# Performance work log

Hardware: AMD Instinct MI355X
Metric: run time of the kernel (lower is better)

The kernel has to match this reference:

```python
import jax, jax.numpy as jnp
import numpy as np

DIM = 128
NUM_HEADS = 2
WS = 8  # window_size


def setup_inputs() -> dict:
    key = jax.random.key(0)
    ks = jax.random.split(key, 8)
    B, C, H, W = 1, DIM, 64, 128  # W must equal DIM (proj acts on last spatial axis)
    w_scale = 1.0 / np.sqrt(DIM)
    return {
        "x": jax.random.normal(ks[0], (B, C, H, W), jnp.float32),
        "wavelet_features": jax.random.normal(ks[1], (B, C, H, W), jnp.float32),
        "Wq": jax.random.normal(ks[2], (DIM, DIM), jnp.float32) * w_scale,
        "bq": jnp.zeros((DIM,), jnp.float32),
        "Wk": jax.random.normal(ks[3], (DIM, DIM), jnp.float32) * w_scale,
        "bk": jnp.zeros((DIM,), jnp.float32),
        "Wv": jax.random.normal(ks[4], (DIM, DIM), jnp.float32) * w_scale,
        "bv": jnp.zeros((DIM,), jnp.float32),
        "Wp": jax.random.normal(ks[5], (DIM, DIM), jnp.float32) * w_scale,
        "bp": jnp.zeros((DIM,), jnp.float32),
    }


def _window_partition(t):
    # 'b c (h wh) (w ww) -> b (h w) (wh ww) c'
    B, C, H, W = t.shape
    h, w = H // WS, W // WS
    t = t.reshape(B, C, h, WS, w, WS)
    t = t.transpose(0, 2, 4, 3, 5, 1)  # B,h,w,wh,ww,C
    return t.reshape(B, h * w, WS * WS, C)


def reference(x, wavelet_features, Wq, bq, Wk, bk, Wv, bv, Wp, bp):
    B, C, H, W = x.shape
    hd = C // NUM_HEADS
    scale = hd ** (-0.5)

    xw = _window_partition(x)                   # [B, nW, ws*ws, C]
    ww = _window_partition(wavelet_features)    # [B, nW, ws*ws, C]

    q = xw @ Wq.T + bq
    k = ww @ Wk.T + bk
    v = ww @ Wv.T + bv

    # NOTE: original code flattens windows+tokens together, so attention is
    # GLOBAL over all N = H*W tokens (window partition is just a permutation).
    N = q.shape[1] * q.shape[2]
    q = q.reshape(B, N, NUM_HEADS, hd).transpose(0, 2, 1, 3)  # [B,h,N,d]
    k = k.reshape(B, N, NUM_HEADS, hd).transpose(0, 2, 1, 3)
    v = v.reshape(B, N, NUM_HEADS, hd).transpose(0, 2, 1, 3)

    attn = jax.nn.softmax(jnp.einsum('bhnd,bhmd->bhnm', q, k) * scale, axis=-1)
    out = jnp.einsum('bhnm,bhmd->bhnd', attn, v)  # [B,h,N,d]
    out = out.transpose(0, 2, 1, 3).reshape(B, N, C)

    # 'b (h w) (wh ww) c -> b c (h wh) (w ww)'
    h, w = H // WS, W // WS
    out = out.reshape(B, h, w, WS, WS, C).transpose(0, 5, 1, 3, 2, 4).reshape(B, C, H, W)

    # Faithful quirk: proj Linear acts on the LAST axis (spatial W == dim).
    out = out @ Wp.T + bp
    return out
```

## Files before the change

### kernel.cpp

```cpp
#include <hip/hip_runtime.h>
#include <stdint.h>

typedef float    f32x4  __attribute__((ext_vector_type(4)));
typedef __bf16   bf16x8 __attribute__((ext_vector_type(8)));
typedef short    s16x8  __attribute__((ext_vector_type(8)));
typedef int      i32x4  __attribute__((ext_vector_type(4)));
typedef unsigned short u16x4 __attribute__((ext_vector_type(4)));

#define DEVINL __device__ __forceinline__

DEVINL unsigned short f2bf(float f) {
  unsigned u = __builtin_bit_cast(unsigned, f);
  return (unsigned short)((u + 0x7fffu + ((u >> 16) & 1u)) >> 16);
}

DEVINL f32x4 mfma16(bf16x8 a, bf16x8 b, f32x4 c) {
  return __builtin_amdgcn_mfma_f32_16x16x32_bf16(a, b, c, 0, 0, 0);
}

DEVINL bf16x8 lds_frag(const unsigned char* p) {
  return __builtin_bit_cast(bf16x8, *(const s16x8*)p);
}

template <int CTRL>
DEVINL float dppf(float x) {
  int xi = __builtin_bit_cast(int, x);
  return __builtin_bit_cast(float, __builtin_amdgcn_update_dpp(xi, xi, CTRL, 0xF, 0xF, true));
}
DEVINL float redmax16(float v) {
  v = fmaxf(v, dppf<0xB1>(v));
  v = fmaxf(v, dppf<0x4E>(v));
  v = fmaxf(v, dppf<0x141>(v));
  v = fmaxf(v, dppf<0x140>(v));
  return v;
}

__global__ __launch_bounds__(256) void prep_w_kernel(
    const float* __restrict__ wq, const float* __restrict__ wk,
    const float* __restrict__ wv, const float* __restrict__ wp,
    unsigned short* __restrict__ wbf) {
  int id = blockIdx.x * 256 + threadIdx.x;
  int m = id >> 12;
  const float* src = (m == 0) ? wq : (m == 1) ? wk : (m == 2) ? wv : wp;
  f32x4 v = ((const f32x4*)src)[id & 4095];
  u16x4 o;
  o[0] = f2bf(v[0]); o[1] = f2bf(v[1]); o[2] = f2bf(v[2]); o[3] = f2bf(v[3]);
  ((u16x4*)wbf)[id] = o;
}

__global__ __launch_bounds__(256) void qkv_kernel(
    const float* __restrict__ x, const float* __restrict__ wav,
    const unsigned short* __restrict__ wbf,
    const float* __restrict__ bq, const float* __restrict__ bk, const float* __restrict__ bv,
    unsigned short* __restrict__ Qb, unsigned short* __restrict__ Kb,
    unsigned short* __restrict__ Vt) {
  __shared__ __align__(16) unsigned char sm[32768];
  const int tid = threadIdx.x;
  const int g = blockIdx.x >> 7;
  const int s0 = (blockIdx.x & 127) * 64;
  const float* srcm = (g == 0) ? x : wav;

  {
    const int c = tid >> 1, half = tid & 1;
    const float* xs = srcm + c * 8192 + s0 + half * 32;
#pragma unroll
    for (int i = 0; i < 8; ++i) {
      f32x4 vx = *(const f32x4*)(xs + i * 4);
#pragma unroll
      for (int j = 0; j < 4; ++j) {
        int s = half * 32 + i * 4 + j;
        int off = (c * 2) ^ ((s & 7) << 4);
        *(unsigned short*)(sm + s * 256 + off) = f2bf(vx[j]);
      }
    }
  }
  __syncthreads();

  const int w = tid >> 6, l = tid & 63, lr = l & 15, lh = l >> 4;
  const int arow = w * 16 + lr;
  const int aswz = (lr & 7) << 4;

  const unsigned char* asrc = sm + arow * 256;
  const unsigned char* wsrc = (const unsigned char*)wbf + g * 32768;
  f32x4 acc[8];
#pragma unroll
  for (int jt = 0; jt < 8; ++jt) acc[jt] = (f32x4){0.f, 0.f, 0.f, 0.f};
#pragma unroll
  for (int ks = 0; ks < 4; ++ks) {
    bf16x8 a = lds_frag(asrc + ((ks * 64 + lh * 16) ^ aswz));
#pragma unroll
    for (int jt = 0; jt < 8; ++jt) {
      bf16x8 bb = __builtin_bit_cast(
          bf16x8, *(const s16x8*)(wsrc + (jt * 16 + lr) * 256 + ks * 64 + lh * 16));
      acc[jt] = mfma16(a, bb, acc[jt]);
    }
  }
  if (g < 2) {
    const float* bias = g ? bk : bq;
    unsigned short* outp = g ? Kb : Qb;
#pragma unroll
    for (int jt = 0; jt < 8; ++jt) {
      float bb = bias[jt * 16 + lr];
#pragma unroll
      for (int r = 0; r < 4; ++r) {
        int row = s0 + w * 16 + lh * 4 + r;
        outp[row * 128 + jt * 16 + lr] = f2bf(acc[jt][r] + bb);
      }
    }
  } else {
    unsigned char* sm2 = sm + 16384;
#pragma unroll
    for (int jt = 0; jt < 8; ++jt) {
      float bb = bv[jt * 16 + lr];
#pragma unroll
      for (int r = 0; r < 4; ++r) {
        int jj = jt * 16 + lr;
        int sl = w * 16 + lh * 4 + r;
        *(unsigned short*)(sm2 + jj * 128 + ((sl * 2) ^ ((jj & 7) << 4))) =
            f2bf(acc[jt][r] + bb);
      }
    }
    __syncthreads();
#pragma unroll
    for (int g2 = 0; g2 < 4; ++g2) {
      int jj = w * 32 + g2 * 8 + (l >> 3);
      s16x8 row = *(const s16x8*)(sm2 + jj * 128 + (((l & 7) * 16) ^ ((jj & 7) << 4)));
      *(s16x8*)(Vt + jj * 8192 + s0 + (l & 7) * 8) = row;
    }
  }
}

__global__ __launch_bounds__(256) void attn_kernel(
    const unsigned short* __restrict__ Qb, const unsigned short* __restrict__ Kb,
    const unsigned short* __restrict__ Vt, float* __restrict__ Opart,
    float* __restrict__ Ml, float* __restrict__ Ll, int NIT) {
  __shared__ __align__(16) unsigned char sm[32768];
  const int tid = threadIdx.x;
  const int bid = blockIdx.x;
  const int sp = bid >> 7, g = bid & 127;
  const int h = g & 1, qb2 = g >> 1;
  const int q0 = qb2 * 128;
  const int t0 = sp * NIT;
  const int w = tid >> 6, l = tid & 63, lr = l & 15, lh = l >> 4;
  const int lswz = (lr & 7) << 4;

  bf16x8 qfA[2], qfB[2];
#pragma unroll
  for (int ks = 0; ks < 2; ++ks) {
    qfA[ks] = __builtin_bit_cast(
        bf16x8, *(const s16x8*)(Qb + (q0 + w * 16 + lr) * 128 + h * 64 + ks * 32 + lh * 8));
    qfB[ks] = __builtin_bit_cast(
        bf16x8, *(const s16x8*)(Qb + (q0 + 64 + w * 16 + lr) * 128 + h * 64 + ks * 32 + lh * 8));
  }

  const s16x8 ones_i = {0x3F80, 0x3F80, 0x3F80, 0x3F80, 0x3F80, 0x3F80, 0x3F80, 0x3F80};
  const bf16x8 onesf = __builtin_bit_cast(bf16x8, ones_i);

  f32x4 accA[4], accB[4];
  float mA[4], lA[4], mB[4], lB[4];
#pragma unroll
  for (int i = 0; i < 4; ++i) {
    accA[i] = (f32x4){0.f,0.f,0.f,0.f}; accB[i] = (f32x4){0.f,0.f,0.f,0.f};
    mA[i] = -1e30f; lA[i] = 0.f; mB[i] = -1e30f; lB[i] = 0.f;
  }

  int srow[2], soff[2], sldsoff[2];
#pragma unroll
  for (int i = 0; i < 2; ++i) {
    int ch = tid + i * 256;
    srow[i] = ch >> 3;
    soff[i] = (ch & 7) * 8;
    sldsoff[i] = srow[i] * 128 + ((soff[i] * 2) ^ ((srow[i] & 7) << 4));
  }

  {
#pragma unroll
    for (int i = 0; i < 2; ++i) {
      i32x4 kv = *(const i32x4*)(Kb + (t0 * 64 + srow[i]) * 128 + h * 64 + soff[i]);
      i32x4 vv = *(const i32x4*)(Vt + (h * 64 + srow[i]) * 8192 + t0 * 64 + soff[i]);
      *(i32x4*)(sm + sldsoff[i]) = kv;
      *(i32x4*)(sm + 8192 + sldsoff[i]) = vv;
    }
  }
  __syncthreads();

  const float sc = 0.18033688011112042f;

  for (int tt = 0; tt < NIT; ++tt) {
    const int t = t0 + tt;
    i32x4 nk[2], nv[2];
    if (tt < NIT - 1) {
#pragma unroll
      for (int i = 0; i < 2; ++i) {
        nk[i] = *(const i32x4*)(Kb + ((t + 1) * 64 + srow[i]) * 128 + h * 64 + soff[i]);
        nv[i] = *(const i32x4*)(Vt + (h * 64 + srow[i]) * 8192 + (t + 1) * 64 + soff[i]);
      }
    }
    const unsigned char* kb = sm;
    const unsigned char* vb = sm + 8192;
    unsigned char* pbA = sm + 16384;
    unsigned char* pbB = sm + 24576;

    f32x4 sA[4], sB[4];
#pragma unroll
    for (int nt = 0; nt < 4; ++nt) { sA[nt] = (f32x4){0.f,0.f,0.f,0.f}; sB[nt] = (f32x4){0.f,0.f,0.f,0.f}; }
#pragma unroll
    for (int ks = 0; ks < 2; ++ks) {
#pragma unroll
      for (int nt = 0; nt < 4; ++nt) {
        bf16x8 kf = lds_frag(kb + (nt * 16 + lr) * 128 + ((ks * 64 + lh * 16) ^ lswz));
        sA[nt] = mfma16(qfA[ks], kf, sA[nt]);
        sB[nt] = mfma16(qfB[ks], kf, sB[nt]);
      }
    }

#pragma unroll
    for (int r = 0; r < 4; ++r) {
      float mx = fmaxf(fmaxf(sA[0][r], sA[1][r]), fmaxf(sA[2][r], sA[3][r]));
      mx = redmax16(mx) * sc;
      float mn = fmaxf(mA[r], mx);
      float al = __builtin_amdgcn_exp2f(mA[r] - mn);
      mA[r] = mn;
      lA[r] *= al;
#pragma unroll
      for (int nt = 0; nt < 4; ++nt)
        sA[nt][r] = __builtin_amdgcn_exp2f(fmaf(sA[nt][r], sc, -mn));
#pragma unroll
      for (int ct = 0; ct < 4; ++ct) accA[ct][r] *= al;
    }
#pragma unroll
    for (int r = 0; r < 4; ++r) {
      float mx = fmaxf(fmaxf(sB[0][r], sB[1][r]), fmaxf(sB[2][r], sB[3][r]));
      mx = redmax16(mx) * sc;
      float mn = fmaxf(mB[r], mx);
      float al = __builtin_amdgcn_exp2f(mB[r] - mn);
      mB[r] = mn;
      lB[r] *= al;
#pragma unroll
      for (int nt = 0; nt < 4; ++nt)
        sB[nt][r] = __builtin_amdgcn_exp2f(fmaf(sB[nt][r], sc, -mn));
#pragma unroll
      for (int ct = 0; ct < 4; ++ct) accB[ct][r] *= al;
    }

    const int qrow = w * 16 + lh * 4;
#pragma unroll
    for (int r = 0; r < 4; r += 2) {
      int qa = qrow + r, qb = qrow + r + 1;
      int swza = (qa & 7) << 4, swzb = (qb & 7) << 4;
#pragma unroll
      for (int nt = 0; nt < 4; ++nt) {
        int koff = (nt * 16 + lr) * 2;
        unsigned u;
        asm("v_cvt_pk_bf16_f32 %0, %1, %2" : "=v"(u) : "v"(sA[nt][r]), "v"(sA[nt][r + 1]));
        *(unsigned short*)(pbA + qa * 128 + (koff ^ swza)) = (unsigned short)u;
        *(unsigned short*)(pbA + qb * 128 + (koff ^ swzb)) = (unsigned short)(u >> 16);
        asm("v_cvt_pk_bf16_f32 %0, %1, %2" : "=v"(u) : "v"(sB[nt][r]), "v"(sB[nt][r + 1]));
        *(unsigned short*)(pbB + qa * 128 + (koff ^ swza)) = (unsigned short)u;
        *(unsigned short*)(pbB + qb * 128 + (koff ^ swzb)) = (unsigned short)(u >> 16);
      }
    }
    asm volatile("s_waitcnt lgkmcnt(0)" ::: "memory");
    __builtin_amdgcn_sched_barrier(0);

    bf16x8 paA[2], paB[2];
#pragma unroll
    for (int ks = 0; ks < 2; ++ks) {
      paA[ks] = lds_frag(pbA + (w * 16 + lr) * 128 + ((ks * 64 + lh * 16) ^ lswz));
      paB[ks] = lds_frag(pbB + (w * 16 + lr) * 128 + ((ks * 64 + lh * 16) ^ lswz));
    }
    f32x4 ltA = (f32x4){0.f,0.f,0.f,0.f}, ltB = (f32x4){0.f,0.f,0.f,0.f};
#pragma unroll
    for (int ks = 0; ks < 2; ++ks) {
      ltA = mfma16(paA[ks], onesf, ltA);
      ltB = mfma16(paB[ks], onesf, ltB);
#pragma unroll
      for (int ct = 0; ct < 4; ++ct) {
        bf16x8 vf = lds_frag(vb + (ct * 16 + lr) * 128 + ((ks * 64 + lh * 16) ^ lswz));
        accA[ct] = mfma16(paA[ks], vf, accA[ct]);
        accB[ct] = mfma16(paB[ks], vf, accB[ct]);
      }
    }
#pragma unroll
    for (int r = 0; r < 4; ++r) { lA[r] += ltA[r]; lB[r] += ltB[r]; }

    __syncthreads();
    if (tt < NIT - 1) {
#pragma unroll
      for (int i = 0; i < 2; ++i) {
        *(i32x4*)(sm + sldsoff[i]) = nk[i];
        *(i32x4*)(sm + 8192 + sldsoff[i]) = nv[i];
      }
    }
    __syncthreads();
  }

  const size_t pbA_i = (size_t)sp * 256 + 4 * qb2 + h;
  const size_t pbB_i = (size_t)sp * 256 + 4 * qb2 + 2 + h;
  float* opA = Opart + pbA_i * 4096;
  float* opB = Opart + pbB_i * 4096;
#pragma unroll
  for (int ct = 0; ct < 4; ++ct) {
#pragma unroll
    for (int r = 0; r < 4; ++r) {
      int q = w * 16 + lh * 4 + r;
      opA[q * 64 + ct * 16 + lr] = accA[ct][r];
      opB[q * 64 + ct * 16 + lr] = accB[ct][r];
    }
  }
  if (lr == 0) {
#pragma unroll
    for (int r = 0; r < 4; ++r) {
      int q = w * 16 + lh * 4 + r;
      Ml[pbA_i * 64 + q] = mA[r];
      Ll[pbA_i * 64 + q] = lA[r];
      Ml[pbB_i * 64 + q] = mB[r];
      Ll[pbB_i * 64 + q] = lB[r];
    }
  }
}

__global__ __launch_bounds__(256) void combine_kernel(
    const float* __restrict__ Opart, const float* __restrict__ Ml,
    const float* __restrict__ Ll, unsigned short* __restrict__ Ot, int S) {
  __shared__ float wgt_s[8][32];
  __shared__ float rinv_s[32];
  __shared__ unsigned short lt[64][34];
  const int bid = blockIdx.x;
  const int hq = bid >> 1, half = bid & 1;
  const int h = hq & 1, q0 = (hq >> 1) * 64;
  const int t = threadIdx.x;

  if (t < 32) {
    int qg = half * 32 + t;
    float m8[8];
    float M = -1e30f;
    for (int sp = 0; sp < S; ++sp) {
      m8[sp] = Ml[(size_t)(sp * 256 + hq) * 64 + qg];
      M = fmaxf(M, m8[sp]);
    }
    float L = 0.f;
    for (int sp = 0; sp < S; ++sp) {
      float wv = __builtin_amdgcn_exp2f(m8[sp] - M);
      wgt_s[sp][t] = wv;
      L += Ll[(size_t)(sp * 256 + hq) * 64 + qg] * wv;
    }
    rinv_s[t] = 1.0f / L;
  }
  __syncthreads();

  const int q = t >> 3;
  const int dc = t & 7;
  const int qg = half * 32 + q;
  f32x4 o0 = (f32x4){0.f,0.f,0.f,0.f}, o1 = (f32x4){0.f,0.f,0.f,0.f};
  for (int sp = 0; sp < S; ++sp) {
    const f32x4* src =
        (const f32x4*)(Opart + (size_t)(sp * 256 + hq) * 4096 + qg * 64 + dc * 8);
    float wv = wgt_s[sp][q];
    o0 += src[0] * wv;
    o1 += src[1] * wv;
  }
  float rinv = rinv_s[q];
#pragma unroll
  for (int j = 0; j < 4; ++j) lt[dc * 8 + j][q] = f2bf(o0[j] * rinv);
#pragma unroll
  for (int j = 0; j < 4; ++j) lt[dc * 8 + 4 + j][q] = f2bf(o1[j] * rinv);
  __syncthreads();

  const int d = t >> 2, q8 = (t & 3) * 8;
  unsigned short tmp[8];
#pragma unroll
  for (int j = 0; j < 8; ++j) tmp[j] = lt[d][q8 + j];
  *(s16x8*)(Ot + (size_t)(h * 64 + d) * 8192 + q0 + half * 32 + q8) = *(s16x8*)tmp;
}

__global__ __launch_bounds__(256) void proj_kernel(
    const unsigned short* __restrict__ Ot, const unsigned short* __restrict__ wbf,
    const float* __restrict__ bp, float* __restrict__ out) {
  __shared__ __align__(16) unsigned char sm[16384];
  const int tid = threadIdx.x;
  const int r0 = blockIdx.x * 64;
#pragma unroll
  for (int i = 0; i < 4; ++i) {
    int chk = tid + 256 * i;
    i32x4 v = *(const i32x4*)(Ot + r0 * 128 + chk * 8);
    int row = chk >> 4, off = (chk & 15) * 16;
    *(i32x4*)(sm + row * 256 + (off ^ ((row & 7) << 4))) = v;
  }
  __syncthreads();
  const int w = tid >> 6, l = tid & 63, lr = l & 15, lh = l >> 4;
  f32x4 acc[8];
#pragma unroll
  for (int jt = 0; jt < 8; ++jt) acc[jt] = (f32x4){0.f, 0.f, 0.f, 0.f};
  const unsigned char* wsrc = (const unsigned char*)wbf + 3 * 32768;
#pragma unroll
  for (int ks = 0; ks < 4; ++ks) {
    bf16x8 a = lds_frag(sm + (w * 16 + lr) * 256 + ((ks * 64 + lh * 16) ^ ((lr & 7) << 4)));
#pragma unroll
    for (int jt = 0; jt < 8; ++jt) {
      bf16x8 bb = __builtin_bit_cast(
          bf16x8, *(const s16x8*)(wsrc + (jt * 16 + lr) * 256 + ks * 64 + lh * 16));
      acc[jt] = mfma16(a, bb, acc[jt]);
    }
  }
#pragma unroll
  for (int jt = 0; jt < 8; ++jt) {
    float bb = bp[jt * 16 + lr];
#pragma unroll
    for (int r = 0; r < 4; ++r)
      out[(r0 + w * 16 + lh * 4 + r) * 128 + jt * 16 + lr] = acc[jt][r] + bb;
  }
}

extern "C" void kernel_launch(void* const* d_in, const int* in_sizes, int n_in,
                              void* d_out, int out_size, void* d_ws, size_t ws_size,
                              hipStream_t stream) {
  const float* x   = (const float*)d_in[0];
  const float* wav = (const float*)d_in[1];
  const float* Wq  = (const float*)d_in[2];
  const float* bq  = (const float*)d_in[3];
  const float* Wk  = (const float*)d_in[4];
  const float* bk  = (const float*)d_in[5];
  const float* Wv  = (const float*)d_in[6];
  const float* bv  = (const float*)d_in[7];
  const float* Wp  = (const float*)d_in[8];
  const float* bp  = (const float*)d_in[9];
  (void)in_sizes; (void)n_in; (void)out_size;

  unsigned char* ws = (unsigned char*)d_ws;
  unsigned short* Qb  = (unsigned short*)(ws);
  unsigned short* Kb  = (unsigned short*)(ws + 2097152);
  unsigned short* Vt  = (unsigned short*)(ws + 4194304);
  unsigned short* Ot  = (unsigned short*)(ws + 6291456);
  unsigned short* Wbf = (unsigned short*)(ws + 8388608);

  const size_t pbase = 8519680;
  int S = 8;
  while (S > 1 && pbase + (size_t)S * 4325376 > ws_size) S >>= 1;
  float* Opart = (float*)(ws + pbase);
  float* Ml    = (float*)(ws + pbase + (size_t)S * 4194304);
  float* Ll    = (float*)(ws + pbase + (size_t)S * 4194304 + (size_t)S * 65536);
  const int NIT = 128 / S;

  prep_w_kernel<<<64, 256, 0, stream>>>(Wq, Wk, Wv, Wp, Wbf);
  qkv_kernel<<<384, 256, 0, stream>>>(x, wav, Wbf, bq, bk, bv, Qb, Kb, Vt);
  attn_kernel<<<128 * S, 256, 0, stream>>>(Qb, Kb, Vt, Opart, Ml, Ll, NIT);
  combine_kernel<<<512, 256, 0, stream>>>(Opart, Ml, Ll, Ot, S);
  proj_kernel<<<128, 256, 0, stream>>>(Ot, Wbf, bp, (float*)d_out);
}
```

Measured before the change: 123.1 us.

## Double key tile to 128 per iteration and alias P buffers over K

The attention loop now handles 128 keys per iteration instead of 64, halving the iteration count and the per-iteration barriers and softmax rescales. The P buffers now overlap the K panel region, which needs an extra barrier after the S computation, and the next-tile global prefetch moves later in the iteration. The larger score tile raises register pressure and LDS use grows to 48KB, which may cut occupancy.

```diff
diff --git a/kernel.cpp b/kernel.cpp
--- a/kernel.cpp
+++ b/kernel.cpp
@@ -134,7 +134,7 @@
     const unsigned short* __restrict__ Qb, const unsigned short* __restrict__ Kb,
     const unsigned short* __restrict__ Vt, float* __restrict__ Opart,
     float* __restrict__ Ml, float* __restrict__ Ll, int NIT) {
-  __shared__ __align__(16) unsigned char sm[32768];
+  __shared__ __align__(16) unsigned char sm[49152];
   const int tid = threadIdx.x;
   const int bid = blockIdx.x;
   const int sp = bid >> 7, g = bid & 127;
@@ -164,22 +164,27 @@
     mA[i] = -1e30f; lA[i] = 0.f; mB[i] = -1e30f; lB[i] = 0.f;
   }
 
-  int srow[2], soff[2], sldsoff[2];
-#pragma unroll
-  for (int i = 0; i < 2; ++i) {
+  int kglob[4], kldsoff[4], vglob[4], vldsoff[4];
+#pragma unroll
+  for (int i = 0; i < 4; ++i) {
     int ch = tid + i * 256;
-    srow[i] = ch >> 3;
-    soff[i] = (ch & 7) * 8;
-    sldsoff[i] = srow[i] * 128 + ((soff[i] * 2) ^ ((srow[i] & 7) << 4));
+    int key = ch >> 3, slot = ch & 7;
+    int kr = key & 63;
+    kldsoff[i] = (key >> 6) * 8192 + kr * 128 + ((slot * 16) ^ ((kr & 7) << 4));
+    kglob[i] = key * 128 + h * 64 + slot * 8;
+    int d = ch >> 4, kslot = ch & 15;
+    vldsoff[i] = 16384 + (kslot >> 3) * 8192 + d * 128 +
+                 (((kslot & 7) * 16) ^ ((d & 7) << 4));
+    vglob[i] = (h * 64 + d) * 8192 + kslot * 8;
   }
 
   {
 #pragma unroll
-    for (int i = 0; i < 2; ++i) {
-      i32x4 kv = *(const i32x4*)(Kb + (t0 * 64 + srow[i]) * 128 + h * 64 + soff[i]);
-      i32x4 vv = *(const i32x4*)(Vt + (h * 64 + srow[i]) * 8192 + t0 * 64 + soff[i]);
-      *(i32x4*)(sm + sldsoff[i]) = kv;
-      *(i32x4*)(sm + 8192 + sldsoff[i]) = vv;
+    for (int i = 0; i < 4; ++i) {
+      i32x4 kv = *(const i32x4*)(Kb + (size_t)t0 * 16384 + kglob[i]);
+      i32x4 vv = *(const i32x4*)(Vt + (size_t)t0 * 128 + vglob[i]);
+      *(i32x4*)(sm + kldsoff[i]) = kv;
+      *(i32x4*)(sm + vldsoff[i]) = vv;
     }
   }
   __syncthreads();
@@ -187,61 +192,54 @@
   const float sc = 0.18033688011112042f;
 
   for (int tt = 0; tt < NIT; ++tt) {
-    const int t = t0 + tt;
-    i32x4 nk[2], nv[2];
-    if (tt < NIT - 1) {
-#pragma unroll
-      for (int i = 0; i < 2; ++i) {
-        nk[i] = *(const i32x4*)(Kb + ((t + 1) * 64 + srow[i]) * 128 + h * 64 + soff[i]);
-        nv[i] = *(const i32x4*)(Vt + (h * 64 + srow[i]) * 8192 + (t + 1) * 64 + soff[i]);
-      }
-    }
-    const unsigned char* kb = sm;
-    const unsigned char* vb = sm + 8192;
-    unsigned char* pbA = sm + 16384;
-    unsigned char* pbB = sm + 24576;
-
-    f32x4 sA[4], sB[4];
-#pragma unroll
-    for (int nt = 0; nt < 4; ++nt) { sA[nt] = (f32x4){0.f,0.f,0.f,0.f}; sB[nt] = (f32x4){0.f,0.f,0.f,0.f}; }
+    f32x4 sA8[8], sB8[8];
+#pragma unroll
+    for (int nt = 0; nt < 8; ++nt) { sA8[nt] = (f32x4){0.f,0.f,0.f,0.f}; sB8[nt] = (f32x4){0.f,0.f,0.f,0.f}; }
 #pragma unroll
     for (int ks = 0; ks < 2; ++ks) {
 #pragma unroll
-      for (int nt = 0; nt < 4; ++nt) {
-        bf16x8 kf = lds_frag(kb + (nt * 16 + lr) * 128 + ((ks * 64 + lh * 16) ^ lswz));
-        sA[nt] = mfma16(qfA[ks], kf, sA[nt]);
-        sB[nt] = mfma16(qfB[ks], kf, sB[nt]);
+      for (int nt = 0; nt < 8; ++nt) {
+        bf16x8 kf = lds_frag(sm + (nt >> 2) * 8192 + ((nt & 3) * 16 + lr) * 128 +
+                             ((ks * 64 + lh * 16) ^ lswz));
+        sA8[nt] = mfma16(qfA[ks], kf, sA8[nt]);
+        sB8[nt] = mfma16(qfB[ks], kf, sB8[nt]);
       }
     }
 
 #pragma unroll
     for (int r = 0; r < 4; ++r) {
-      float mx = fmaxf(fmaxf(sA[0][r], sA[1][r]), fmaxf(sA[2][r], sA[3][r]));
+      float mx = sA8[0][r];
+#pragma unroll
+      for (int nt = 1; nt < 8; ++nt) mx = fmaxf(mx, sA8[nt][r]);
       mx = redmax16(mx) * sc;
       float mn = fmaxf(mA[r], mx);
       float al = __builtin_amdgcn_exp2f(mA[r] - mn);
       mA[r] = mn;
       lA[r] *= al;
 #pragma unroll
-      for (int nt = 0; nt < 4; ++nt)
-        sA[nt][r] = __builtin_amdgcn_exp2f(fmaf(sA[nt][r], sc, -mn));
+      for (int nt = 0; nt < 8; ++nt)
+        sA8[nt][r] = __builtin_amdgcn_exp2f(fmaf(sA8[nt][r], sc, -mn));
 #pragma unroll
       for (int ct = 0; ct < 4; ++ct) accA[ct][r] *= al;
     }
 #pragma unroll
     for (int r = 0; r < 4; ++r) {
-      float mx = fmaxf(fmaxf(sB[0][r], sB[1][r]), fmaxf(sB[2][r], sB[3][r]));
+      float mx = sB8[0][r];
+#pragma unroll
+      for (int nt = 1; nt < 8; ++nt) mx = fmaxf(mx, sB8[nt][r]);
       mx = redmax16(mx) * sc;
       float mn = fmaxf(mB[r], mx);
       float al = __builtin_amdgcn_exp2f(mB[r] - mn);
       mB[r] = mn;
       lB[r] *= al;
 #pragma unroll
-      for (int nt = 0; nt < 4; ++nt)
-        sB[nt][r] = __builtin_amdgcn_exp2f(fmaf(sB[nt][r], sc, -mn));
+      for (int nt = 0; nt < 8; ++nt)
+        sB8[nt][r] = __builtin_amdgcn_exp2f(fmaf(sB8[nt][r], sc, -mn));
 #pragma unroll
       for (int ct = 0; ct < 4; ++ct) accB[ct][r] *= al;
     }
+
+    __syncthreads();
 
     const int qrow = w * 16 + lh * 4;
 #pragma unroll
@@ -249,34 +247,47 @@
       int qa = qrow + r, qb = qrow + r + 1;
       int swza = (qa & 7) << 4, swzb = (qb & 7) << 4;
 #pragma unroll
-      for (int nt = 0; nt < 4; ++nt) {
-        int koff = (nt * 16 + lr) * 2;
+      for (int nt = 0; nt < 8; ++nt) {
+        int pbase = (nt >> 2) * 8192;
+        int koff = (nt & 3) * 32 + lr * 2;
         unsigned u;
-        asm("v_cvt_pk_bf16_f32 %0, %1, %2" : "=v"(u) : "v"(sA[nt][r]), "v"(sA[nt][r + 1]));
-        *(unsigned short*)(pbA + qa * 128 + (koff ^ swza)) = (unsigned short)u;
-        *(unsigned short*)(pbA + qb * 128 + (koff ^ swzb)) = (unsigned short)(u >> 16);
-        asm("v_cvt_pk_bf16_f32 %0, %1, %2" : "=v"(u) : "v"(sB[nt][r]), "v"(sB[nt][r + 1]));
-        *(unsigned short*)(pbB + qa * 128 + (koff ^ swza)) = (unsigned short)u;
-        *(unsigned short*)(pbB + qb * 128 + (koff ^ swzb)) = (unsigned short)(u >> 16);
+        asm("v_cvt_pk_bf16_f32 %0, %1, %2" : "=v"(u) : "v"(sA8[nt][r]), "v"(sA8[nt][r + 1]));
+        *(unsigned short*)(sm + pbase + qa * 128 + (koff ^ swza)) = (unsigned short)u;
+        *(unsigned short*)(sm + pbase + qb * 128 + (koff ^ swzb)) = (unsigned short)(u >> 16);
+        asm("v_cvt_pk_bf16_f32 %0, %1, %2" : "=v"(u) : "v"(sB8[nt][r]), "v"(sB8[nt][r + 1]));
+        *(unsigned short*)(sm + 32768 + pbase + qa * 128 + (koff ^ swza)) = (unsigned short)u;
+        *(unsigned short*)(sm + 32768 + pbase + qb * 128 + (koff ^ swzb)) = (unsigned short)(u >> 16);
       }
     }
     asm volatile("s_waitcnt lgkmcnt(0)" ::: "memory");
     __builtin_amdgcn_sched_barrier(0);
 
-    bf16x8 paA[2], paB[2];
-#pragma unroll
-    for (int ks = 0; ks < 2; ++ks) {
-      paA[ks] = lds_frag(pbA + (w * 16 + lr) * 128 + ((ks * 64 + lh * 16) ^ lswz));
-      paB[ks] = lds_frag(pbB + (w * 16 + lr) * 128 + ((ks * 64 + lh * 16) ^ lswz));
+    i32x4 nk[4], nv[4];
+    if (tt < NIT - 1) {
+#pragma unroll
+      for (int i = 0; i < 4; ++i) {
+        nk[i] = *(const i32x4*)(Kb + (size_t)(t0 + tt + 1) * 16384 + kglob[i]);
+        nv[i] = *(const i32x4*)(Vt + (size_t)(t0 + tt + 1) * 128 + vglob[i]);
+      }
+    }
+
+    bf16x8 paA[4], paB[4];
+#pragma unroll
+    for (int ks = 0; ks < 4; ++ks) {
+      int poff = (ks >> 1) * 8192 + (w * 16 + lr) * 128 + (((ks & 1) * 64 + lh * 16) ^ lswz);
+      paA[ks] = lds_frag(sm + poff);
+      paB[ks] = lds_frag(sm + 32768 + poff);
     }
     f32x4 ltA = (f32x4){0.f,0.f,0.f,0.f}, ltB = (f32x4){0.f,0.f,0.f,0.f};
 #pragma unroll
-    for (int ks = 0; ks < 2; ++ks) {
+    for (int ks = 0; ks < 4; ++ks) {
       ltA = mfma16(paA[ks], onesf, ltA);
       ltB = mfma16(paB[ks], onesf, ltB);
+      const unsigned char* vpan = sm + 16384 + (ks >> 1) * 8192;
 #pragma unroll
       for (int ct = 0; ct < 4; ++ct) {
-        bf16x8 vf = lds_frag(vb + (ct * 16 + lr) * 128 + ((ks * 64 + lh * 16) ^ lswz));
+        bf16x8 vf = lds_frag(vpan + (ct * 16 + lr) * 128 +
+                             (((ks & 1) * 64 + lh * 16) ^ lswz));
         accA[ct] = mfma16(paA[ks], vf, accA[ct]);
         accB[ct] = mfma16(paB[ks], vf, accB[ct]);
       }
@@ -287,9 +298,9 @@
     __syncthreads();
     if (tt < NIT - 1) {
 #pragma unroll
-      for (int i = 0; i < 2; ++i) {
-        *(i32x4*)(sm + sldsoff[i]) = nk[i];
-        *(i32x4*)(sm + 8192 + sldsoff[i]) = nv[i];
+      for (int i = 0; i < 4; ++i) {
+        *(i32x4*)(sm + kldsoff[i]) = nk[i];
+        *(i32x4*)(sm + vldsoff[i]) = nv[i];
       }
     }
     __syncthreads();
@@ -440,7 +451,7 @@
   float* Opart = (float*)(ws + pbase);
   float* Ml    = (float*)(ws + pbase + (size_t)S * 4194304);
   float* Ll    = (float*)(ws + pbase + (size_t)S * 4194304 + (size_t)S * 65536);
-  const int NIT = 128 / S;
+  const int NIT = 64 / S;
 
   prep_w_kernel<<<64, 256, 0, stream>>>(Wq, Wk, Wv, Wp, Wbf);
   qkv_kernel<<<384, 256, 0, stream>>>(x, wav, Wbf, bq, bk, bv, Qb, Kb, Vt);
```

Result: slower. 130.6 us (+6.1%).
